# Optimization experiments

Measured on AMD Instinct MI355X. Metric: run time of the kernel, lower is better.

## Reference

```python
import jax, jax.numpy as jnp
import numpy as np


def sparsemax(z):
    # z: [..., E] -> sparse probability simplex projection (Martins & Astudillo 2016).
    E = z.shape[-1]
    z_sorted = -jnp.sort(-z, axis=-1)                 # descending
    z_cum = jnp.cumsum(z_sorted, axis=-1)
    k = jnp.arange(1, E + 1, dtype=z.dtype)
    support = (1.0 + k * z_sorted) > z_cum            # [..., E] bool
    k_z = jnp.sum(support, axis=-1, keepdims=True)    # support size >= 1
    tau_sum = jnp.take_along_axis(z_cum, k_z.astype(jnp.int32) - 1, axis=-1)
    tau = (tau_sum - 1.0) / k_z.astype(z.dtype)
    return jnp.maximum(z - tau, 0.0)


def setup_inputs() -> dict:
    key = jax.random.key(0)
    ks = jax.random.split(key, 6)
    B, S, D_IN, D_OUT, E, R = 8, 2048, 4096, 4096, 8, 16
    x = jax.random.normal(ks[0], (B, S, D_IN), dtype=jnp.float32)
    W_base = jax.random.normal(ks[1], (D_OUT, D_IN), dtype=jnp.float32) * (D_IN ** -0.5)
    b_base = jax.random.normal(ks[2], (D_OUT,), dtype=jnp.float32) * 0.01
    W_router = jax.random.normal(ks[3], (E, D_IN), dtype=jnp.float32) * (D_IN ** -0.5)
    b_router = jnp.zeros((E,), dtype=jnp.float32)
    lora_A = jax.random.normal(ks[4], (E, D_IN, R), dtype=jnp.float32) * (D_IN ** -0.5)
    lora_B = jnp.zeros((E, R, D_OUT), dtype=jnp.float32)  # standard LoRA zero-init on B
    return {"x": x, "W_base": W_base, "b_base": b_base,
            "W_router": W_router, "b_router": b_router,
            "lora_A": lora_A, "lora_B": lora_B}


def reference(x, W_base, b_base, W_router, b_router, lora_A, lora_B):
    # Frozen base projection: [B,S,D_in] @ [D_in,D_out]
    base_out = jnp.einsum('bsd,od->bso', x, W_base) + b_base
    # Sparsegen (sparsemax) router over experts
    logits = jnp.einsum('bsd,ed->bse', x, W_router) + b_router
    weights = sparsemax(logits)                       # [B,S,E], mostly-sparse
    # LoRA experts: low-rank path per expert, summed with token-dependent weights
    h = jnp.einsum('bsd,edr->bser', x, lora_A)        # [B,S,E,R]
    expert_out = jnp.einsum('bser,bse,ero->bso', h, weights, lora_B)
    return base_out + expert_out
```

## Files before the change

### kernel.cpp

```cpp
#include <hip/hip_runtime.h>
#include <hip/hip_bf16.h>

#define M_TOK 16384
#define DK    4096
#define DN    4096
#define NE    8
#define NR    16
#define ERC   128
#define RAC   160
#define NT_MAIN 128
#define NT_ALL  132

typedef __attribute__((ext_vector_type(8))) short bfrag;
typedef __attribute__((ext_vector_type(4))) float f32x4;

__device__ __forceinline__ unsigned short f2bf(float f) {
  unsigned u = __builtin_bit_cast(unsigned, f);
  unsigned rounding = 0x7FFFu + ((u >> 16) & 1u);
  u += rounding;
  return (unsigned short)(u >> 16);
}

__device__ __forceinline__ void load_lds16(const void* g, void* l) {
  __builtin_amdgcn_global_load_lds(
      (__attribute__((address_space(1))) void*)(g),
      (__attribute__((address_space(3))) void*)(l), 16, 0, 0);
}

__global__ void k_cvt(const float* __restrict__ in, unsigned short* __restrict__ out, long n4) {
  long i = (long)blockIdx.x * blockDim.x + threadIdx.x;
  long stride = (long)gridDim.x * blockDim.x;
  for (; i < n4; i += stride) {
    float4 v = reinterpret_cast<const float4*>(in)[i];
    ushort4 o;
    o.x = f2bf(v.x); o.y = f2bf(v.y); o.z = f2bf(v.z); o.w = f2bf(v.w);
    reinterpret_cast<ushort4*>(out)[i] = o;
  }
}

__global__ void k_build_ra(const float* __restrict__ Wr, const float* __restrict__ lA,
                           unsigned short* __restrict__ RA) {
  int idx = blockIdx.x * 256 + threadIdx.x;
  if (idx >= RAC * DK) return;
  int c = idx >> 12;
  int k = idx & (DK - 1);
  float v = 0.f;
  if (c < NE) {
    v = Wr[c * DK + k];
  } else if (c < NE + ERC) {
    int er = c - NE;
    int e = er >> 4, r = er & 15;
    v = lA[((long)e * DK + k) * NR + r];
  }
  RA[idx] = f2bf(v);
}

__global__ void k_build_bt(const float* __restrict__ lB, unsigned short* __restrict__ BT) {
  int idx = blockIdx.x * 256 + threadIdx.x;
  if (idx >= DN * ERC) return;
  int n = idx >> 7;
  int kp = idx & 127;
  BT[idx] = f2bf(lB[(long)kp * DN + n]);
}

__global__ __launch_bounds__(256, 2)
void k_small_fused(const float* __restrict__ x, const unsigned short* __restrict__ RA,
                   unsigned short* __restrict__ Xb, const float* __restrict__ b_router,
                   unsigned short* __restrict__ Gout) {
  __shared__ unsigned short At[64 * 64];
  __shared__ unsigned short Bt[RAC * 64];
  __shared__ float Hl[64][160];
  __shared__ float Wl[64][NE];
  int m0 = blockIdx.x * 64;
  int tid = threadIdx.x;
  int lane = tid & 63, wid = tid >> 6;
  int wr = wid >> 1, wc = wid & 1;
  int l16 = lane & 15, lhi = lane >> 4;
  f32x4 acc[2][5] = {};
  int row = tid >> 2, c16 = (tid & 3) * 16;
  int byteoff = tid * 16;
  for (int k0 = 0; k0 < DK; k0 += 64) {
    const float* xs = x + (long)(m0 + row) * DK + k0 + c16;
    float4 v0 = *(const float4*)(xs);
    float4 v1 = *(const float4*)(xs + 4);
    float4 v2 = *(const float4*)(xs + 8);
    float4 v3 = *(const float4*)(xs + 12);
    bfrag lo, hi;
    lo[0] = (short)f2bf(v0.x); lo[1] = (short)f2bf(v0.y);
    lo[2] = (short)f2bf(v0.z); lo[3] = (short)f2bf(v0.w);
    lo[4] = (short)f2bf(v1.x); lo[5] = (short)f2bf(v1.y);
    lo[6] = (short)f2bf(v1.z); lo[7] = (short)f2bf(v1.w);
    hi[0] = (short)f2bf(v2.x); hi[1] = (short)f2bf(v2.y);
    hi[2] = (short)f2bf(v2.z); hi[3] = (short)f2bf(v2.w);
    hi[4] = (short)f2bf(v3.x); hi[5] = (short)f2bf(v3.y);
    hi[6] = (short)f2bf(v3.z); hi[7] = (short)f2bf(v3.w);
    unsigned short* xb = Xb + (long)(m0 + row) * DK + k0 + c16;
    *(bfrag*)xb = lo;
    *(bfrag*)(xb + 8) = hi;
    *(bfrag*)&At[row * 64 + c16] = lo;
    *(bfrag*)&At[row * 64 + c16 + 8] = hi;
#pragma unroll
    for (int r = 0; r < 5; r++) {
      int off = r * 4096 + byteoff;
      int rrow = off >> 7, colb = off & 127;
      load_lds16((const char*)RA + ((long)rrow * DK + k0) * 2 + colb, (char*)Bt + off);
    }
    __syncthreads();
#pragma unroll
    for (int kk = 0; kk < 2; kk++) {
      bfrag a[2], b[5];
#pragma unroll
      for (int m = 0; m < 2; m++)
        a[m] = *(const bfrag*)&At[(wr * 32 + m * 16 + l16) * 64 + kk * 32 + lhi * 8];
#pragma unroll
      for (int n = 0; n < 5; n++)
        b[n] = *(const bfrag*)&Bt[(wc * 80 + n * 16 + l16) * 64 + kk * 32 + lhi * 8];
#pragma unroll
      for (int m = 0; m < 2; m++)
#pragma unroll
        for (int n = 0; n < 5; n++)
          acc[m][n] = __builtin_amdgcn_mfma_f32_16x16x32_bf16(a[m], b[n], acc[m][n], 0, 0, 0);
    }
    __syncthreads();
  }
#pragma unroll
  for (int m = 0; m < 2; m++)
#pragma unroll
    for (int n = 0; n < 5; n++) {
      int col = wc * 80 + n * 16 + l16;
      int trow = wr * 32 + m * 16 + lhi * 4;
#pragma unroll
      for (int j = 0; j < 4; j++)
        Hl[trow + j][col] = acc[m][n][j];
    }
  __syncthreads();
  if (tid < 64) {
    float z[NE], zs[NE];
#pragma unroll
    for (int e = 0; e < NE; e++) { z[e] = Hl[tid][e] + b_router[e]; zs[e] = z[e]; }
#pragma unroll
    for (int i = 1; i < NE; i++) {
      float key = zs[i];
      int j = i - 1;
      while (j >= 0 && zs[j] < key) { zs[j + 1] = zs[j]; j--; }
      zs[j + 1] = key;
    }
    float cums[NE];
    float cum = 0.f;
#pragma unroll
    for (int j = 0; j < NE; j++) { cum += zs[j]; cums[j] = cum; }
    int kz = 0;
#pragma unroll
    for (int j = 0; j < NE; j++)
      if (1.f + (float)(j + 1) * zs[j] > cums[j]) kz = j + 1;
    float tau = (cums[kz - 1] - 1.f) / (float)kz;
#pragma unroll
    for (int e = 0; e < NE; e++)
      Wl[tid][e] = fmaxf(z[e] - tau, 0.f);
  }
  __syncthreads();
  for (int idx = tid; idx < 64 * ERC; idx += 256) {
    int tk = idx >> 7, er = idx & 127;
    Gout[(long)(m0 + tk) * ERC + er] = f2bf(Wl[tk][er >> 4] * Hl[tk][NE + er]);
  }
}

struct KtArgs {
  const unsigned short *pXA0, *pXA1, *pWB0, *pWB1, *pGA0, *pGA1, *pTB0, *pTB1;
  int soffA0, soffA1, soffB0, soffB1;
  int wr, wc, l16, swslot;
};

template<bool STAGE, int VMB>
__device__ __forceinline__ void ktile_body(int t, unsigned short* lds, const KtArgs& A,
                                           f32x4 (&acc)[8][4]) {
  unsigned short* s = lds + (t & 3) * 16384;
  bfrag bfr[4], al[4], ah[4];
#pragma unroll
  for (int n = 0; n < 4; n++)
    bfr[n] = *(const bfrag*)&s[8192 + (A.wc * 64 + n * 16 + A.l16) * 32 + A.swslot];
#pragma unroll
  for (int m = 0; m < 4; m++)
    al[m] = *(const bfrag*)&s[(A.wr * 128 + m * 16 + A.l16) * 32 + A.swslot];
  if constexpr (STAGE) {
    int u = t + 3;
    unsigned short* d = lds + (u & 3) * 16384;
    if (u < NT_MAIN) {
      load_lds16(A.pXA0 + (long)u * 32, d + A.soffA0);
      load_lds16(A.pXA1 + (long)u * 32, d + A.soffA1);
    } else {
      long v = u - NT_MAIN;
      load_lds16(A.pGA0 + v * 32, d + A.soffA0);
      load_lds16(A.pGA1 + v * 32, d + A.soffA1);
    }
  }
  asm volatile("s_barrier\n\ts_waitcnt lgkmcnt(0)" ::: "memory");
  __builtin_amdgcn_sched_barrier(0);
  __builtin_amdgcn_s_setprio(1);
#pragma unroll
  for (int m = 0; m < 4; m++)
#pragma unroll
    for (int n = 0; n < 4; n++)
      acc[m][n] = __builtin_amdgcn_mfma_f32_16x16x32_bf16(al[m], bfr[n], acc[m][n], 0, 0, 0);
  __builtin_amdgcn_s_setprio(0);
#pragma unroll
  for (int m = 0; m < 4; m++)
    ah[m] = *(const bfrag*)&s[(A.wr * 128 + 64 + m * 16 + A.l16) * 32 + A.swslot];
  if constexpr (STAGE) {
    int u = t + 3;
    unsigned short* d = lds + (u & 3) * 16384;
    if (u < NT_MAIN) {
      load_lds16(A.pWB0 + (long)u * 32, d + A.soffB0);
      load_lds16(A.pWB1 + (long)u * 32, d + A.soffB1);
    } else {
      long v = u - NT_MAIN;
      load_lds16(A.pTB0 + v * 32, d + A.soffB0);
      load_lds16(A.pTB1 + v * 32, d + A.soffB1);
    }
  }
  asm volatile("s_barrier\n\ts_waitcnt lgkmcnt(0)" ::: "memory");
  __builtin_amdgcn_sched_barrier(0);
  __builtin_amdgcn_s_setprio(1);
#pragma unroll
  for (int m = 0; m < 4; m++)
#pragma unroll
    for (int n = 0; n < 4; n++)
      acc[4 + m][n] = __builtin_amdgcn_mfma_f32_16x16x32_bf16(ah[m], bfr[n], acc[4 + m][n], 0, 0, 0);
  __builtin_amdgcn_s_setprio(0);
  if constexpr (VMB == 8)      asm volatile("s_waitcnt vmcnt(8)\n\ts_barrier" ::: "memory");
  else if constexpr (VMB == 4) asm volatile("s_waitcnt vmcnt(4)\n\ts_barrier" ::: "memory");
  else if constexpr (VMB == 0) asm volatile("s_waitcnt vmcnt(0)\n\ts_barrier" ::: "memory");
}

__global__ __launch_bounds__(512, 2)
void k_gemm_main(const unsigned short* __restrict__ X, const unsigned short* __restrict__ W,
                 const unsigned short* __restrict__ G, const unsigned short* __restrict__ BT,
                 const float* __restrict__ bias, float* __restrict__ out) {
  __shared__ unsigned short lds[4 * 16384];
  int bid = blockIdx.x;
  int swz = (bid & 7) * 128 + (bid >> 3);
  int bm = swz >> 4, bn = swz & 15;
  int m0 = bm * 256, n0 = bn * 256;
  int tid = threadIdx.x;
  int lane = tid & 63, wid = tid >> 6;

  KtArgs A;
  A.wr = wid >> 2; A.wc = wid & 3;
  A.l16 = lane & 15;
  int lhi = lane >> 4;
  A.swslot = (lhi ^ ((A.l16 >> 1) & 3)) * 8;
  int r0 = tid >> 2;
  int c8 = (((tid & 3) ^ ((tid >> 3) & 3)) * 8);
  A.pXA0 = X + (long)(m0 + r0) * DK + c8;
  A.pXA1 = X + (long)(m0 + 128 + r0) * DK + c8;
  A.pWB0 = W + (long)(n0 + r0) * DK + c8;
  A.pWB1 = W + (long)(n0 + 128 + r0) * DK + c8;
  A.pGA0 = G + (long)(m0 + r0) * ERC + c8;
  A.pGA1 = G + (long)(m0 + 128 + r0) * ERC + c8;
  A.pTB0 = BT + (long)(n0 + r0) * ERC + c8;
  A.pTB1 = BT + (long)(n0 + 128 + r0) * ERC + c8;
  A.soffA0 = tid * 8;
  A.soffA1 = 4096 + tid * 8;
  A.soffB0 = 8192 + tid * 8;
  A.soffB1 = 12288 + tid * 8;

  f32x4 acc[8][4] = {};

#pragma unroll
  for (int u = 0; u < 3; u++) {
    unsigned short* d = lds + u * 16384;
    load_lds16(A.pXA0 + (long)u * 32, d + A.soffA0);
    load_lds16(A.pXA1 + (long)u * 32, d + A.soffA1);
    load_lds16(A.pWB0 + (long)u * 32, d + A.soffB0);
    load_lds16(A.pWB1 + (long)u * 32, d + A.soffB1);
  }
  asm volatile("s_waitcnt vmcnt(8)\n\ts_barrier" ::: "memory");

  for (int t = 0; t <= 128; t++)
    ktile_body<true, 8>(t, lds, A, acc);
  ktile_body<false, 4>(129, lds, A, acc);
  ktile_body<false, 0>(130, lds, A, acc);
  ktile_body<false, -1>(131, lds, A, acc);

#pragma unroll
  for (int n = 0; n < 4; n++) {
    int col = n0 + A.wc * 64 + n * 16 + A.l16;
    float bv = bias[col];
#pragma unroll
    for (int m = 0; m < 8; m++) {
      int row = m0 + A.wr * 128 + m * 16 + lhi * 4;
#pragma unroll
      for (int j = 0; j < 4; j++)
        out[(long)(row + j) * DN + col] = acc[m][n][j] + bv;
    }
  }
}

extern "C" void kernel_launch(void* const* d_in, const int* in_sizes, int n_in,
                              void* d_out, int out_size, void* d_ws, size_t ws_size,
                              hipStream_t stream) {
  const float* x        = (const float*)d_in[0];
  const float* W_base   = (const float*)d_in[1];
  const float* b_base   = (const float*)d_in[2];
  const float* W_router = (const float*)d_in[3];
  const float* b_router = (const float*)d_in[4];
  const float* lora_A   = (const float*)d_in[5];
  const float* lora_B   = (const float*)d_in[6];
  float* out = (float*)d_out;

  char* ws = (char*)d_ws;
  unsigned short* Xb = (unsigned short*)ws;
  unsigned short* Wb = (unsigned short*)(ws + 134217728L);
  unsigned short* RA = (unsigned short*)(ws + 167772160L);
  unsigned short* BT = (unsigned short*)(ws + 169082880L);
  unsigned short* G  = (unsigned short*)(ws + 180617216L);

  hipLaunchKernelGGL(k_cvt, dim3(2048), dim3(256), 0, stream, W_base, Wb, (long)DN * DK / 4);
  hipLaunchKernelGGL(k_build_ra, dim3((RAC * DK + 255) / 256), dim3(256), 0, stream,
                     W_router, lora_A, RA);
  hipLaunchKernelGGL(k_build_bt, dim3((DN * ERC + 255) / 256), dim3(256), 0, stream, lora_B, BT);
  hipLaunchKernelGGL(k_small_fused, dim3(M_TOK / 64), dim3(256), 0, stream,
                     x, RA, Xb, b_router, G);
  hipLaunchKernelGGL(k_gemm_main, dim3((M_TOK / 256) * (DN / 256)), dim3(512), 0, stream,
                     Xb, Wb, G, BT, b_base, out);
}
```

Measured before the change: 674.0 us.

## Restructure GEMM main loop to BK=64 double-buffered tiles with split-half staging

The main fused GEMM now uses 64-wide K tiles with two LDS buffers instead of 32-wide K tiles with four buffers. This halves the number of k-iterations, and each tile is split into four MFMA quadrants with interleaved LDS reads and half-tile global-to-LDS staging. The XOR swizzle is widened to 8 slots to match the 64-element rows. The aim is to cut per-tile barrier and wait overhead and overlap staging with compute at finer granularity, at the cost of more barriers per tile, a shallower prefetch depth and more fragment registers.

```diff
diff --git a/kernel.cpp b/kernel.cpp
--- a/kernel.cpp
+++ b/kernel.cpp
@@ -8,8 +8,7 @@
 #define NR    16
 #define ERC   128
 #define RAC   160
-#define NT_MAIN 128
-#define NT_ALL  132
+#define NT64  66
 
 typedef __attribute__((ext_vector_type(8))) short bfrag;
 typedef __attribute__((ext_vector_type(4))) float f32x4;
@@ -166,69 +165,105 @@
 }
 
 struct KtArgs {
-  const unsigned short *pXA0, *pXA1, *pWB0, *pWB1, *pGA0, *pGA1, *pTB0, *pTB1;
-  int soffA0, soffA1, soffB0, soffB1;
-  int wr, wc, l16, swslot;
+  const unsigned short *pX, *pW, *pG, *pT;
+  int aB, bB, sw0, sw1, tid8;
 };
 
-template<bool STAGE, int VMB>
-__device__ __forceinline__ void ktile_body(int t, unsigned short* lds, const KtArgs& A,
-                                           f32x4 (&acc)[8][4]) {
-  unsigned short* s = lds + (t & 3) * 16384;
-  bfrag bfr[4], al[4], ah[4];
-#pragma unroll
-  for (int n = 0; n < 4; n++)
-    bfr[n] = *(const bfrag*)&s[8192 + (A.wc * 64 + n * 16 + A.l16) * 32 + A.swslot];
-#pragma unroll
-  for (int m = 0; m < 4; m++)
-    al[m] = *(const bfrag*)&s[(A.wr * 128 + m * 16 + A.l16) * 32 + A.swslot];
-  if constexpr (STAGE) {
-    int u = t + 3;
-    unsigned short* d = lds + (u & 3) * 16384;
-    if (u < NT_MAIN) {
-      load_lds16(A.pXA0 + (long)u * 32, d + A.soffA0);
-      load_lds16(A.pXA1 + (long)u * 32, d + A.soffA1);
-    } else {
-      long v = u - NT_MAIN;
-      load_lds16(A.pGA0 + v * 32, d + A.soffA0);
-      load_lds16(A.pGA1 + v * 32, d + A.soffA1);
-    }
-  }
-  asm volatile("s_barrier\n\ts_waitcnt lgkmcnt(0)" ::: "memory");
+__device__ __forceinline__ void stage_half(unsigned short* lds, const KtArgs& A,
+                                           int u, int arr, int h) {
+  unsigned short* dst = lds + arr * 32768 + (u & 1) * 16384 + h * 8192 + A.tid8;
+  if (u < 64) {
+    const unsigned short* s = (arr ? A.pW : A.pX) + (long)(h * 128) * DK + (long)u * 64;
+    load_lds16(s, dst);
+    load_lds16(s + (long)64 * DK, dst + 4096);
+  } else {
+    const unsigned short* s = (arr ? A.pT : A.pG) + (long)(h * 128) * ERC + (long)(u - 64) * 64;
+    load_lds16(s, dst);
+    load_lds16(s + (long)64 * ERC, dst + 4096);
+  }
+}
+
+template<bool AHI, bool T2, int VMB>
+__device__ __forceinline__ void ktile(int t, unsigned short* lds, const KtArgs& A,
+                                      f32x4 (&acc)[8][4]) {
+  unsigned short* L = lds + (t & 1) * 16384;
+  bfrag bl[4], bh[4], al[8], ah[8];
+#pragma unroll
+  for (int nf = 0; nf < 2; nf++)
+#pragma unroll
+    for (int kk = 0; kk < 2; kk++)
+      bl[nf * 2 + kk] = *(const bfrag*)&L[A.bB + nf * 1024 + (kk ? A.sw1 : A.sw0)];
+#pragma unroll
+  for (int f = 0; f < 4; f++)
+#pragma unroll
+    for (int kk = 0; kk < 2; kk++)
+      al[f * 2 + kk] = *(const bfrag*)&L[A.aB + f * 1024 + (kk ? A.sw1 : A.sw0)];
+  if constexpr (AHI) stage_half(lds, A, t + 1, 0, 1);
+  asm volatile("s_waitcnt lgkmcnt(8)" ::: "memory");
+  __builtin_amdgcn_s_barrier();
+  asm volatile("s_waitcnt lgkmcnt(0)" ::: "memory");
   __builtin_amdgcn_sched_barrier(0);
   __builtin_amdgcn_s_setprio(1);
 #pragma unroll
-  for (int m = 0; m < 4; m++)
-#pragma unroll
-    for (int n = 0; n < 4; n++)
-      acc[m][n] = __builtin_amdgcn_mfma_f32_16x16x32_bf16(al[m], bfr[n], acc[m][n], 0, 0, 0);
+  for (int f = 0; f < 4; f++)
+#pragma unroll
+    for (int nf = 0; nf < 2; nf++)
+#pragma unroll
+      for (int kk = 0; kk < 2; kk++)
+        acc[f][nf] = __builtin_amdgcn_mfma_f32_16x16x32_bf16(al[f * 2 + kk], bl[nf * 2 + kk], acc[f][nf], 0, 0, 0);
   __builtin_amdgcn_s_setprio(0);
-#pragma unroll
-  for (int m = 0; m < 4; m++)
-    ah[m] = *(const bfrag*)&s[(A.wr * 128 + 64 + m * 16 + A.l16) * 32 + A.swslot];
-  if constexpr (STAGE) {
-    int u = t + 3;
-    unsigned short* d = lds + (u & 3) * 16384;
-    if (u < NT_MAIN) {
-      load_lds16(A.pWB0 + (long)u * 32, d + A.soffB0);
-      load_lds16(A.pWB1 + (long)u * 32, d + A.soffB1);
-    } else {
-      long v = u - NT_MAIN;
-      load_lds16(A.pTB0 + v * 32, d + A.soffB0);
-      load_lds16(A.pTB1 + v * 32, d + A.soffB1);
-    }
-  }
-  asm volatile("s_barrier\n\ts_waitcnt lgkmcnt(0)" ::: "memory");
+  __builtin_amdgcn_s_barrier();
+#pragma unroll
+  for (int nf = 0; nf < 2; nf++)
+#pragma unroll
+    for (int kk = 0; kk < 2; kk++)
+      bh[nf * 2 + kk] = *(const bfrag*)&L[A.bB + (2 + nf) * 1024 + (kk ? A.sw1 : A.sw0)];
+  __builtin_amdgcn_s_barrier();
+  asm volatile("s_waitcnt lgkmcnt(0)" ::: "memory");
   __builtin_amdgcn_sched_barrier(0);
   __builtin_amdgcn_s_setprio(1);
 #pragma unroll
-  for (int m = 0; m < 4; m++)
-#pragma unroll
-    for (int n = 0; n < 4; n++)
-      acc[4 + m][n] = __builtin_amdgcn_mfma_f32_16x16x32_bf16(ah[m], bfr[n], acc[4 + m][n], 0, 0, 0);
+  for (int f = 0; f < 4; f++)
+#pragma unroll
+    for (int nf = 0; nf < 2; nf++)
+#pragma unroll
+      for (int kk = 0; kk < 2; kk++)
+        acc[f][2 + nf] = __builtin_amdgcn_mfma_f32_16x16x32_bf16(al[f * 2 + kk], bh[nf * 2 + kk], acc[f][2 + nf], 0, 0, 0);
   __builtin_amdgcn_s_setprio(0);
-  if constexpr (VMB == 8)      asm volatile("s_waitcnt vmcnt(8)\n\ts_barrier" ::: "memory");
-  else if constexpr (VMB == 4) asm volatile("s_waitcnt vmcnt(4)\n\ts_barrier" ::: "memory");
+  __builtin_amdgcn_s_barrier();
+#pragma unroll
+  for (int f = 0; f < 4; f++)
+#pragma unroll
+    for (int kk = 0; kk < 2; kk++)
+      ah[f * 2 + kk] = *(const bfrag*)&L[A.aB + (4 + f) * 1024 + (kk ? A.sw1 : A.sw0)];
+  if constexpr (T2) stage_half(lds, A, t + 2, 1, 0);
+  __builtin_amdgcn_s_barrier();
+  asm volatile("s_waitcnt lgkmcnt(0)" ::: "memory");
+  __builtin_amdgcn_sched_barrier(0);
+  __builtin_amdgcn_s_setprio(1);
+#pragma unroll
+  for (int f = 0; f < 4; f++)
+#pragma unroll
+    for (int nf = 0; nf < 2; nf++)
+#pragma unroll
+      for (int kk = 0; kk < 2; kk++)
+        acc[4 + f][nf] = __builtin_amdgcn_mfma_f32_16x16x32_bf16(ah[f * 2 + kk], bl[nf * 2 + kk], acc[4 + f][nf], 0, 0, 0);
+  __builtin_amdgcn_s_setprio(0);
+  __builtin_amdgcn_s_barrier();
+  if constexpr (T2) {
+    stage_half(lds, A, t + 2, 1, 1);
+    stage_half(lds, A, t + 2, 0, 0);
+  }
+  __builtin_amdgcn_s_setprio(1);
+#pragma unroll
+  for (int f = 0; f < 4; f++)
+#pragma unroll
+    for (int nf = 0; nf < 2; nf++)
+#pragma unroll
+      for (int kk = 0; kk < 2; kk++)
+        acc[4 + f][2 + nf] = __builtin_amdgcn_mfma_f32_16x16x32_bf16(ah[f * 2 + kk], bh[nf * 2 + kk], acc[4 + f][2 + nf], 0, 0, 0);
+  __builtin_amdgcn_s_setprio(0);
+  if constexpr (VMB == 6)      asm volatile("s_waitcnt vmcnt(6)\n\ts_barrier" ::: "memory");
   else if constexpr (VMB == 0) asm volatile("s_waitcnt vmcnt(0)\n\ts_barrier" ::: "memory");
 }
 
@@ -236,62 +271,55 @@
 void k_gemm_main(const unsigned short* __restrict__ X, const unsigned short* __restrict__ W,
                  const unsigned short* __restrict__ G, const unsigned short* __restrict__ BT,
                  const float* __restrict__ bias, float* __restrict__ out) {
-  __shared__ unsigned short lds[4 * 16384];
+  __shared__ unsigned short lds[65536];
   int bid = blockIdx.x;
   int swz = (bid & 7) * 128 + (bid >> 3);
   int bm = swz >> 4, bn = swz & 15;
   int m0 = bm * 256, n0 = bn * 256;
   int tid = threadIdx.x;
   int lane = tid & 63, wid = tid >> 6;
+  int wr = wid >> 2, wc = wid & 3;
+  int l16 = lane & 15, lhi = lane >> 4;
 
   KtArgs A;
-  A.wr = wid >> 2; A.wc = wid & 3;
-  A.l16 = lane & 15;
-  int lhi = lane >> 4;
-  A.swslot = (lhi ^ ((A.l16 >> 1) & 3)) * 8;
-  int r0 = tid >> 2;
-  int c8 = (((tid & 3) ^ ((tid >> 3) & 3)) * 8);
-  A.pXA0 = X + (long)(m0 + r0) * DK + c8;
-  A.pXA1 = X + (long)(m0 + 128 + r0) * DK + c8;
-  A.pWB0 = W + (long)(n0 + r0) * DK + c8;
-  A.pWB1 = W + (long)(n0 + 128 + r0) * DK + c8;
-  A.pGA0 = G + (long)(m0 + r0) * ERC + c8;
-  A.pGA1 = G + (long)(m0 + 128 + r0) * ERC + c8;
-  A.pTB0 = BT + (long)(n0 + r0) * ERC + c8;
-  A.pTB1 = BT + (long)(n0 + 128 + r0) * ERC + c8;
-  A.soffA0 = tid * 8;
-  A.soffA1 = 4096 + tid * 8;
-  A.soffB0 = 8192 + tid * 8;
-  A.soffB1 = 12288 + tid * 8;
+  A.sw0 = (lhi ^ (l16 & 7)) * 8;
+  A.sw1 = ((4 + lhi) ^ (l16 & 7)) * 8;
+  A.aB = wr * 8192 + l16 * 64;
+  A.bB = 32768 + (wc >> 1) * 8192 + ((wc & 1) * 64 + l16) * 64;
+  A.tid8 = tid * 8;
+  int swz8 = ((tid & 7) ^ ((tid >> 3) & 7)) * 8;
+  int r0 = tid >> 3;
+  A.pX = X + (long)(m0 + r0) * DK + swz8;
+  A.pW = W + (long)(n0 + r0) * DK + swz8;
+  A.pG = G + (long)(m0 + r0) * ERC + swz8;
+  A.pT = BT + (long)(n0 + r0) * ERC + swz8;
 
   f32x4 acc[8][4] = {};
 
-#pragma unroll
-  for (int u = 0; u < 3; u++) {
-    unsigned short* d = lds + u * 16384;
-    load_lds16(A.pXA0 + (long)u * 32, d + A.soffA0);
-    load_lds16(A.pXA1 + (long)u * 32, d + A.soffA1);
-    load_lds16(A.pWB0 + (long)u * 32, d + A.soffB0);
-    load_lds16(A.pWB1 + (long)u * 32, d + A.soffB1);
-  }
-  asm volatile("s_waitcnt vmcnt(8)\n\ts_barrier" ::: "memory");
-
-  for (int t = 0; t <= 128; t++)
-    ktile_body<true, 8>(t, lds, A, acc);
-  ktile_body<false, 4>(129, lds, A, acc);
-  ktile_body<false, 0>(130, lds, A, acc);
-  ktile_body<false, -1>(131, lds, A, acc);
-
-#pragma unroll
-  for (int n = 0; n < 4; n++) {
-    int col = n0 + A.wc * 64 + n * 16 + A.l16;
+  stage_half(lds, A, 0, 0, 0);
+  stage_half(lds, A, 0, 1, 0);
+  stage_half(lds, A, 0, 1, 1);
+  stage_half(lds, A, 0, 0, 1);
+  stage_half(lds, A, 1, 0, 0);
+  stage_half(lds, A, 1, 1, 0);
+  stage_half(lds, A, 1, 1, 1);
+  asm volatile("s_waitcnt vmcnt(6)\n\ts_barrier" ::: "memory");
+
+  for (int t = 0; t < 64; t++)
+    ktile<true, true, 6>(t, lds, A, acc);
+  ktile<true, false, 0>(64, lds, A, acc);
+  ktile<false, false, -1>(65, lds, A, acc);
+
+#pragma unroll
+  for (int nf = 0; nf < 4; nf++) {
+    int col = n0 + wc * 64 + nf * 16 + l16;
     float bv = bias[col];
 #pragma unroll
-    for (int m = 0; m < 8; m++) {
-      int row = m0 + A.wr * 128 + m * 16 + lhi * 4;
+    for (int f = 0; f < 8; f++) {
+      int row = m0 + wr * 128 + f * 16 + lhi * 4;
 #pragma unroll
       for (int j = 0; j < 4; j++)
-        out[(long)(row + j) * DN + col] = acc[m][n][j] + bv;
+        out[(long)(row + j) * DN + col] = acc[f][nf][j] + bv;
     }
   }
 }
```

Result: faster. 634.4 us (-5.9%).

## Switch GEMM main loop to 3-stage buffer with single barrier per k-tile

Applied to the files above, without the earlier changes.

Replaces the 4-stage LDS ring with prefetch distance 3, which used two half-tile phases each fenced by a barrier, with a 3-stage ring and prefetch distance 2. Each k-tile now loads all eight A fragments at once, issues 32 MFMAs back to back, and then stages the next tile into the slot freed by the previous iteration. This removes one barrier and one lgkmcnt wait per tile and cuts LDS use, which may help occupancy. In exchange there is less latency hiding for global loads, more fragment registers are live at once, and the LDS reads no longer overlap with MFMA.

```diff
diff --git a/kernel.cpp b/kernel.cpp
--- a/kernel.cpp
+++ b/kernel.cpp
@@ -171,64 +171,41 @@
   int wr, wc, l16, swslot;
 };
 
-template<bool STAGE, int VMB>
-__device__ __forceinline__ void ktile_body(int t, unsigned short* lds, const KtArgs& A,
-                                           f32x4 (&acc)[8][4]) {
-  unsigned short* s = lds + (t & 3) * 16384;
-  bfrag bfr[4], al[4], ah[4];
+template<bool STG, int VMB>
+__device__ __forceinline__ void ktile_body(int t, int s, int su, unsigned short* lds,
+                                           const KtArgs& A, f32x4 (&acc)[8][4]) {
+  unsigned short* L = lds + s * 16384;
+  bfrag b[4], a[8];
 #pragma unroll
   for (int n = 0; n < 4; n++)
-    bfr[n] = *(const bfrag*)&s[8192 + (A.wc * 64 + n * 16 + A.l16) * 32 + A.swslot];
-#pragma unroll
-  for (int m = 0; m < 4; m++)
-    al[m] = *(const bfrag*)&s[(A.wr * 128 + m * 16 + A.l16) * 32 + A.swslot];
-  if constexpr (STAGE) {
-    int u = t + 3;
-    unsigned short* d = lds + (u & 3) * 16384;
+    b[n] = *(const bfrag*)&L[8192 + (A.wc * 64 + n * 16 + A.l16) * 32 + A.swslot];
+#pragma unroll
+  for (int m = 0; m < 8; m++)
+    a[m] = *(const bfrag*)&L[(A.wr * 128 + m * 16 + A.l16) * 32 + A.swslot];
+  __builtin_amdgcn_s_setprio(1);
+#pragma unroll
+  for (int m = 0; m < 8; m++)
+#pragma unroll
+    for (int n = 0; n < 4; n++)
+      acc[m][n] = __builtin_amdgcn_mfma_f32_16x16x32_bf16(a[m], b[n], acc[m][n], 0, 0, 0);
+  __builtin_amdgcn_s_setprio(0);
+  if constexpr (STG) {
+    int u = t + 2;
+    unsigned short* d = lds + su * 16384;
     if (u < NT_MAIN) {
       load_lds16(A.pXA0 + (long)u * 32, d + A.soffA0);
       load_lds16(A.pXA1 + (long)u * 32, d + A.soffA1);
+      load_lds16(A.pWB0 + (long)u * 32, d + A.soffB0);
+      load_lds16(A.pWB1 + (long)u * 32, d + A.soffB1);
     } else {
       long v = u - NT_MAIN;
       load_lds16(A.pGA0 + v * 32, d + A.soffA0);
       load_lds16(A.pGA1 + v * 32, d + A.soffA1);
-    }
-  }
-  asm volatile("s_barrier\n\ts_waitcnt lgkmcnt(0)" ::: "memory");
-  __builtin_amdgcn_sched_barrier(0);
-  __builtin_amdgcn_s_setprio(1);
-#pragma unroll
-  for (int m = 0; m < 4; m++)
-#pragma unroll
-    for (int n = 0; n < 4; n++)
-      acc[m][n] = __builtin_amdgcn_mfma_f32_16x16x32_bf16(al[m], bfr[n], acc[m][n], 0, 0, 0);
-  __builtin_amdgcn_s_setprio(0);
-#pragma unroll
-  for (int m = 0; m < 4; m++)
-    ah[m] = *(const bfrag*)&s[(A.wr * 128 + 64 + m * 16 + A.l16) * 32 + A.swslot];
-  if constexpr (STAGE) {
-    int u = t + 3;
-    unsigned short* d = lds + (u & 3) * 16384;
-    if (u < NT_MAIN) {
-      load_lds16(A.pWB0 + (long)u * 32, d + A.soffB0);
-      load_lds16(A.pWB1 + (long)u * 32, d + A.soffB1);
-    } else {
-      long v = u - NT_MAIN;
       load_lds16(A.pTB0 + v * 32, d + A.soffB0);
       load_lds16(A.pTB1 + v * 32, d + A.soffB1);
     }
   }
-  asm volatile("s_barrier\n\ts_waitcnt lgkmcnt(0)" ::: "memory");
-  __builtin_amdgcn_sched_barrier(0);
-  __builtin_amdgcn_s_setprio(1);
-#pragma unroll
-  for (int m = 0; m < 4; m++)
-#pragma unroll
-    for (int n = 0; n < 4; n++)
-      acc[4 + m][n] = __builtin_amdgcn_mfma_f32_16x16x32_bf16(ah[m], bfr[n], acc[4 + m][n], 0, 0, 0);
-  __builtin_amdgcn_s_setprio(0);
-  if constexpr (VMB == 8)      asm volatile("s_waitcnt vmcnt(8)\n\ts_barrier" ::: "memory");
-  else if constexpr (VMB == 4) asm volatile("s_waitcnt vmcnt(4)\n\ts_barrier" ::: "memory");
+  if constexpr (VMB == 4)      asm volatile("s_waitcnt vmcnt(4)\n\ts_barrier" ::: "memory");
   else if constexpr (VMB == 0) asm volatile("s_waitcnt vmcnt(0)\n\ts_barrier" ::: "memory");
 }
 
@@ -236,7 +213,7 @@
 void k_gemm_main(const unsigned short* __restrict__ X, const unsigned short* __restrict__ W,
                  const unsigned short* __restrict__ G, const unsigned short* __restrict__ BT,
                  const float* __restrict__ bias, float* __restrict__ out) {
-  __shared__ unsigned short lds[4 * 16384];
+  __shared__ unsigned short lds[3 * 16384];
   int bid = blockIdx.x;
   int swz = (bid & 7) * 128 + (bid >> 3);
   int bm = swz >> 4, bn = swz & 15;
@@ -267,20 +244,24 @@
   f32x4 acc[8][4] = {};
 
 #pragma unroll
-  for (int u = 0; u < 3; u++) {
+  for (int u = 0; u < 2; u++) {
     unsigned short* d = lds + u * 16384;
     load_lds16(A.pXA0 + (long)u * 32, d + A.soffA0);
     load_lds16(A.pXA1 + (long)u * 32, d + A.soffA1);
     load_lds16(A.pWB0 + (long)u * 32, d + A.soffB0);
     load_lds16(A.pWB1 + (long)u * 32, d + A.soffB1);
   }
-  asm volatile("s_waitcnt vmcnt(8)\n\ts_barrier" ::: "memory");
-
-  for (int t = 0; t <= 128; t++)
-    ktile_body<true, 8>(t, lds, A, acc);
-  ktile_body<false, 4>(129, lds, A, acc);
-  ktile_body<false, 0>(130, lds, A, acc);
-  ktile_body<false, -1>(131, lds, A, acc);
+  asm volatile("s_waitcnt vmcnt(4)\n\ts_barrier" ::: "memory");
+
+  int s = 0;
+  for (int t = 0; t < 130; t++) {
+    int su = (s >= 1) ? s - 1 : 2;
+    ktile_body<true, 4>(t, s, su, lds, A, acc);
+    s = (s == 2) ? 0 : s + 1;
+  }
+  ktile_body<false, 0>(130, s, 0, lds, A, acc);
+  s = (s == 2) ? 0 : s + 1;
+  ktile_body<false, -1>(131, s, 0, lds, A, acc);
 
 #pragma unroll
   for (int n = 0; n < 4; n++) {
```

After: 687.9 us. 1.02x slower.
